# Kernel tuning notes

Hardware: AMD Instinct MI355X
Metric: run time of the kernel (lower is better)

## Reference

```python
import jax, jax.numpy as jnp
import numpy as np

N, E, D, EDIM, L, H = 50000, 800000, 128, 16, 3, 8


def setup_inputs() -> dict:
    key = jax.random.key(0)
    ks = jax.random.split(key, 16)
    inner = (L + 1) * D  # concat of input + 3 GCN layer outputs
    return {
        "x": jax.random.normal(ks[0], (N, D), jnp.float32),
        "edge_index": jax.random.randint(ks[1], (2, E), 0, N),
        "edge_attr": jax.random.normal(ks[2], (E, EDIM), jnp.float32),
        "dag_edge_index": jax.random.randint(ks[3], (2, E), 0, N),
        "W_v": jax.random.normal(ks[4], (D, D), jnp.float32) * 0.05,
        "W_qk": jax.random.normal(ks[5], (D, 2 * D), jnp.float32) * 0.05,
        "gcn_W": jax.random.normal(ks[6], (L, D, D), jnp.float32) * 0.05,
        "gcn_b": jnp.zeros((L, D), jnp.float32),
        "gcn_root": jax.random.normal(ks[7], (L, D), jnp.float32) * 0.05,
        "gcn_We": jax.random.normal(ks[8], (L, EDIM, D), jnp.float32) * 0.05,
        "gcn_be": jnp.zeros((L, D), jnp.float32),
        "bn_gamma": jnp.ones((inner,), jnp.float32),
        "bn_beta": jnp.zeros((inner,), jnp.float32),
        "W_se": jax.random.normal(ks[9], (inner, D), jnp.float32) * 0.05,
        "b_se": jnp.zeros((D,), jnp.float32),
        "W_out": jax.random.normal(ks[10], (D, D), jnp.float32) * 0.05,
        "b_out": jnp.zeros((D,), jnp.float32),
    }


def reference(x, edge_index, edge_attr, dag_edge_index, W_v, W_qk, gcn_W, gcn_b,
              gcn_root, gcn_We, gcn_be, bn_gamma, bn_beta, W_se, b_se, W_out, b_out):
    n = x.shape[0]
    row, col = edge_index[0], edge_index[1]  # source j, target i

    def gcn_layer(h, Wl, bl, root, We, be):
        h = h @ Wl + bl                                   # [N, D]
        e = edge_attr @ We + be                           # [E, D]
        deg = jax.ops.segment_sum(jnp.ones(row.shape[0], h.dtype), row, num_segments=n) + 1.0
        dis = deg ** -0.5
        norm = dis[row] * dis[col]                        # [E]
        msg = norm[:, None] * jax.nn.relu(h[row] + e)     # gather + per-edge transform
        agg = jax.ops.segment_sum(msg, col, num_segments=n)  # scatter-add at target
        return agg + jax.nn.relu(h + root) / deg[:, None]

    # StructureExtractor: 3 GCN layers, concat skip features
    xs = [x]
    h = x
    for i in range(gcn_W.shape[0]):
        h = jax.nn.relu(gcn_layer(h, gcn_W[i], gcn_b[i], gcn_root[i], gcn_We[i], gcn_be[i]))
        xs.append(h)
    xc = jnp.concatenate(xs, axis=-1)                     # [N, 4D]
    mu = xc.mean(0)
    var = xc.var(0)
    xc = (xc - mu) / jnp.sqrt(var + 1e-5) * bn_gamma + bn_beta  # BatchNorm1d (batch stats)
    x_struct = xc @ W_se + b_se                           # [N, D]

    # sparse multi-head attention over dag_rr_edge_index
    v = x @ W_v
    qk = x_struct @ W_qk
    d = x.shape[1]
    qk_src_tbl, qk_dst_tbl = qk[:, :d], qk[:, d:]         # chunk(2): (qk_j, qk_i)
    hd = d // H
    scale = hd ** -0.5
    src, dst = dag_edge_index[0], dag_edge_index[1]
    qj = qk_src_tbl[src].reshape(-1, H, hd)
    qi = qk_dst_tbl[dst].reshape(-1, H, hd)
    logits = (qi * qj).sum(-1) * scale                    # [E, H]
    m = jax.ops.segment_max(logits, dst, num_segments=n)
    p = jnp.exp(logits - m[dst])
    s = jax.ops.segment_sum(p, dst, num_segments=n)
    attn = p / s[dst]                                     # per-destination softmax
    vj = v[src].reshape(-1, H, hd)
    out = jax.ops.segment_sum(vj * attn[..., None], dst, num_segments=n).reshape(-1, d)
    return out @ W_out + b_out
```

## Files before the change

### kernel.cpp

```cpp
#include <hip/hip_runtime.h>

#define D 128
#define EDIMC 16
#define GCAP 64

typedef __attribute__((ext_vector_type(8))) short short8v;
typedef __attribute__((ext_vector_type(4))) float f32x4;
typedef __attribute__((ext_vector_type(2))) float f32x2;
typedef __attribute__((ext_vector_type(2))) _Float16 h16x2;

__device__ __forceinline__ float asf(unsigned u){ union{unsigned u; float f;} v; v.u = u; return v.f; }
__device__ __forceinline__ unsigned asu(float f){ union{float f; unsigned u;} v; v.f = f; return v.u; }
__device__ __forceinline__ unsigned short f2bf(float f){
    unsigned u = asu(f);
    unsigned r = (u + 0x7fffu + ((u >> 16) & 1u)) >> 16;
    return (unsigned short)r;
}
__device__ __forceinline__ unsigned packbf(float lo, float hi){
    return (unsigned)f2bf(lo) | ((unsigned)f2bf(hi) << 16);
}
__device__ __forceinline__ unsigned packh(float a, float b){
    union{ h16x2 h; unsigned u; } v;
    v.h = (h16x2){(_Float16)a, (_Float16)b};
    return v.u;
}
__device__ __forceinline__ h16x2 ash2(unsigned u){ union{unsigned u; h16x2 h;} v; v.u = u; return v.h; }

__global__ __launch_bounds__(256) void prep_all(
    const int* __restrict__ row, const int* __restrict__ col,
    const int* __restrict__ asrc_in, const int* __restrict__ adst,
    int E, int N, int gE, int gX, int L,
    const float* __restrict__ eattr, const float* __restrict__ x,
    const float* __restrict__ gW, const float* __restrict__ Wv,
    const float* __restrict__ Wqk, const float* __restrict__ Wout,
    const float* __restrict__ gWe, const float* __restrict__ bse,
    const float* __restrict__ Wse,
    int* __restrict__ cr, int* __restrict__ curg, int* __restrict__ curd,
    int2* __restrict__ gslot, int* __restrict__ asrcS, unsigned* __restrict__ eattrh,
    unsigned* __restrict__ xbf, unsigned* __restrict__ xc,
    unsigned short* __restrict__ gWt, unsigned short* __restrict__ Wvt,
    unsigned short* __restrict__ Woutt, unsigned* __restrict__ wpk,
    float* __restrict__ WseWqk, float* __restrict__ bconst)
{
    int b = blockIdx.x, tid = threadIdx.x;
    if(b < gE){
        int e = b*256 + tid;
        if(e >= E) return;
        const float4* s4 = (const float4*)(eattr + (size_t)e*EDIMC);
        float4 a = s4[0], bb = s4[1], cc2 = s4[2], d = s4[3];
        unsigned* dst8 = eattrh + (size_t)e*8;
        dst8[0] = packh(a.x, a.y);    dst8[1] = packh(a.z, a.w);
        dst8[2] = packh(bb.x, bb.y);  dst8[3] = packh(bb.z, bb.w);
        dst8[4] = packh(cc2.x, cc2.y);dst8[5] = packh(cc2.z, cc2.w);
        dst8[6] = packh(d.x, d.y);    dst8[7] = packh(d.z, d.w);
        int r = row[e], c = col[e];
        atomicAdd(&cr[r], 1);
        int pg = atomicAdd(&curg[c], 1);
        if(pg < GCAP) gslot[c*GCAP + pg] = make_int2(r, e);
        int s2 = asrc_in[e], d2 = adst[e];
        int pd = atomicAdd(&curd[d2], 1);
        if(pd < GCAP) asrcS[d2*GCAP + pd] = s2;
    } else if(b < gE + gX){
        int idx = (b - gE)*256 + tid;
        if(idx >= N*64) return;
        int i = idx >> 6, c2 = idx & 63;
        float a = x[(size_t)i*128 + c2*2], bb = x[(size_t)i*128 + c2*2 + 1];
        unsigned p = packbf(a, bb);
        xbf[idx] = p;
        xc[(size_t)i*256 + c2] = p;
    } else {
        int wb = b - gE - gX;
        int j = tid;
        if(wb < 384){
            int l = wb >> 7, k = wb & 127;
            if(j < 128) gWt[(size_t)l*16384 + (size_t)j*128 + k] = f2bf(gW[(size_t)l*16384 + (size_t)k*128 + j]);
        } else if(wb < 512){
            int k = wb - 384;
            if(j < 128) Wvt[(size_t)j*128 + k] = f2bf(Wv[(size_t)k*128 + j]);
        } else if(wb < 640){
            int k = wb - 512;
            if(j < 128) Woutt[(size_t)j*128 + k] = f2bf(Wout[(size_t)k*128 + j]);
        } else if(wb < 664){
            int t = wb - 640; int l = t >> 3, kk = t & 7;
            if(j < 128){
                const float* W = gWe + (size_t)l*EDIMC*D;
                wpk[(size_t)l*1024 + kk*128 + j] = packh(W[(size_t)(2*kk)*D + j], W[(size_t)(2*kk+1)*D + j]);
            }
        } else if(wb < 1176){
            int k = wb - 664;
            float acc = 0.f;
            #pragma unroll 4
            for(int c = 0; c < 128; c++)
                acc += Wse[(size_t)k*128 + c] * Wqk[(size_t)c*256 + j];
            WseWqk[(size_t)k*256 + j] = acc;
        } else {
            float acc = 0.f;
            #pragma unroll 4
            for(int c = 0; c < 128; c++)
                acc += bse[c] * Wqk[(size_t)c*256 + j];
            bconst[j] = acc;
        }
    }
}

__global__ void deg_fin2(const int* __restrict__ cr, float* __restrict__ deg,
                         float* __restrict__ dis, int N){
    int i = blockIdx.x*blockDim.x + threadIdx.x;
    if(i < N){ float d = (float)cr[i] + 1.0f; deg[i] = d; dis[i] = rsqrtf(d); }
}

template<int OUT>
__global__ __launch_bounds__(256) void gemm_lds(
    const unsigned short* __restrict__ A, const unsigned short* __restrict__ Bt,
    const float* __restrict__ bias, void* __restrict__ Cout,
    int M, int K, int Nc)
{
    __shared__ unsigned short As[128*64];
    __shared__ unsigned short Bs[128*64];
    int tid = threadIdx.x;
    int lane = tid & 63;
    int wid = tid >> 6;
    int bm = blockIdx.y*128, bn = blockIdx.x*128;
    int wr = (wid >> 1)*64, wc = (wid & 1)*64;
    int lr = lane & 15, kg = lane >> 4;
    f32x4 acc[4][4];
    #pragma unroll
    for(int i = 0; i < 4; i++)
        #pragma unroll
        for(int j = 0; j < 4; j++) acc[i][j] = (f32x4){0.f,0.f,0.f,0.f};

    for(int k0 = 0; k0 < K; k0 += 64){
        #pragma unroll
        for(int i = 0; i < 4; i++){
            int q = tid + 256*i;
            int row = q >> 3, c8 = (q & 7)*8;
            int ar = bm + row; if(ar >= M) ar = M - 1;
            *(short8v*)&As[row*64 + c8] = *(const short8v*)&A[(size_t)ar*K + k0 + c8];
            *(short8v*)&Bs[row*64 + c8] = *(const short8v*)&Bt[(size_t)(bn + row)*K + k0 + c8];
        }
        __syncthreads();
        #pragma unroll
        for(int kk = 0; kk < 2; kk++){
            short8v a[4], b[4];
            #pragma unroll
            for(int i = 0; i < 4; i++)
                a[i] = *(const short8v*)&As[(wr + i*16 + lr)*64 + kk*32 + kg*8];
            #pragma unroll
            for(int j = 0; j < 4; j++)
                b[j] = *(const short8v*)&Bs[(wc + j*16 + lr)*64 + kk*32 + kg*8];
            #pragma unroll
            for(int i = 0; i < 4; i++)
                #pragma unroll
                for(int j = 0; j < 4; j++)
                    acc[i][j] = __builtin_amdgcn_mfma_f32_16x16x32_bf16(a[i], b[j], acc[i][j], 0, 0, 0);
        }
        __syncthreads();
    }
    #pragma unroll
    for(int j = 0; j < 4; j++){
        int col = bn + wc + j*16 + lr;
        float bs = bias ? bias[col] : 0.f;
        #pragma unroll
        for(int i = 0; i < 4; i++){
            int rbase = bm + wr + i*16 + kg*4;
            #pragma unroll
            for(int r = 0; r < 4; r++){
                int rw = rbase + r;
                if(rw < M){
                    float val = acc[i][j][r] + bs;
                    if(OUT == 1)
                        ((unsigned short*)Cout)[(size_t)rw*Nc + col] = f2bf(val);
                    else if(OUT == 2)
                        ((_Float16*)Cout)[(size_t)rw*Nc + col] = (_Float16)val;
                    else
                        ((float*)Cout)[(size_t)rw*Nc + col] = val;
                }
            }
        }
    }
}

__device__ __forceinline__ void edge_acc5(
    uint4 ea0, uint4 ea1, unsigned hu, float nm,
    const unsigned* __restrict__ w0, const unsigned* __restrict__ w1,
    float be0, float be1, float& a0, float& a1)
{
    float ev0 = be0, ev1 = be1;
    unsigned ea[8] = {ea0.x, ea0.y, ea0.z, ea0.w, ea1.x, ea1.y, ea1.z, ea1.w};
    #pragma unroll
    for(int kk = 0; kk < 8; kk++){
        ev0 = __builtin_amdgcn_fdot2(ash2(ea[kk]), ash2(w0[kk]), ev0, false);
        ev1 = __builtin_amdgcn_fdot2(ash2(ea[kk]), ash2(w1[kk]), ev1, false);
    }
    float sx = fmaxf(asf(hu << 16) + ev0, 0.f);
    float sy = fmaxf(asf(hu & 0xffff0000u) + ev1, 0.f);
    a0 += nm*sx; a1 += nm*sy;
}

__global__ __launch_bounds__(256) void gcn_gather_v7(
    const unsigned* __restrict__ hlin, const int* __restrict__ curg,
    const int2* __restrict__ gslot, const unsigned* __restrict__ eattrh,
    const float* __restrict__ dis, const unsigned* __restrict__ wpk_l,
    const float* __restrict__ be, const float* __restrict__ root,
    const float* __restrict__ deg,
    unsigned* __restrict__ xc, unsigned* __restrict__ hcur, int blk, int N)
{
    int lane = threadIdx.x & 63;
    int node = __builtin_amdgcn_readfirstlane((int)((blockIdx.x*blockDim.x + threadIdx.x) >> 6));
    if(node >= N) return;
    unsigned w0[8], w1[8];
    const uint2* wp2 = (const uint2*)wpk_l;
    #pragma unroll
    for(int kk = 0; kk < 8; kk++){
        uint2 t = wp2[(size_t)kk*64 + lane];
        w0[kk] = t.x; w1[kk] = t.y;
    }
    f32x2 be2 = ((const f32x2*)be)[lane];
    f32x2 rt2 = ((const f32x2*)root)[lane];
    float disn = dis[node];
    int s0 = node*GCAP;
    int s1 = s0 + min(curg[node], GCAP);
    float a0 = 0.f, a1 = 0.f;
    int s = s0;
    for(; s + 4 <= s1; s += 4){
        int2 sl0 = gslot[s+0], sl1 = gslot[s+1], sl2 = gslot[s+2], sl3 = gslot[s+3];
        float d0 = dis[sl0.x], d1 = dis[sl1.x], d2 = dis[sl2.x], d3 = dis[sl3.x];
        unsigned h0 = hlin[(size_t)sl0.x*64 + lane];
        unsigned h1 = hlin[(size_t)sl1.x*64 + lane];
        unsigned h2 = hlin[(size_t)sl2.x*64 + lane];
        unsigned h3 = hlin[(size_t)sl3.x*64 + lane];
        uint4 e00 = *(const uint4*)(eattrh + (size_t)sl0.y*8);
        uint4 e01 = *(const uint4*)(eattrh + (size_t)sl0.y*8 + 4);
        uint4 e10 = *(const uint4*)(eattrh + (size_t)sl1.y*8);
        uint4 e11 = *(const uint4*)(eattrh + (size_t)sl1.y*8 + 4);
        uint4 e20 = *(const uint4*)(eattrh + (size_t)sl2.y*8);
        uint4 e21 = *(const uint4*)(eattrh + (size_t)sl2.y*8 + 4);
        uint4 e30 = *(const uint4*)(eattrh + (size_t)sl3.y*8);
        uint4 e31 = *(const uint4*)(eattrh + (size_t)sl3.y*8 + 4);
        edge_acc5(e00, e01, h0, d0*disn, w0, w1, be2.x, be2.y, a0, a1);
        edge_acc5(e10, e11, h1, d1*disn, w0, w1, be2.x, be2.y, a0, a1);
        edge_acc5(e20, e21, h2, d2*disn, w0, w1, be2.x, be2.y, a0, a1);
        edge_acc5(e30, e31, h3, d3*disn, w0, w1, be2.x, be2.y, a0, a1);
    }
    for(; s < s1; s++){
        int2 sl0 = gslot[s];
        float d0 = dis[sl0.x];
        unsigned h0 = hlin[(size_t)sl0.x*64 + lane];
        uint4 e00 = *(const uint4*)(eattrh + (size_t)sl0.y*8);
        uint4 e01 = *(const uint4*)(eattrh + (size_t)sl0.y*8 + 4);
        edge_acc5(e00, e01, h0, d0*disn, w0, w1, be2.x, be2.y, a0, a1);
    }
    unsigned hlu = hlin[(size_t)node*64 + lane];
    float hlx = asf(hlu << 16), hly = asf(hlu & 0xffff0000u);
    float dinv = 1.f/deg[node];
    float v0 = fmaxf(a0 + fmaxf(hlx + rt2.x, 0.f)*dinv, 0.f);
    float v1 = fmaxf(a1 + fmaxf(hly + rt2.y, 0.f)*dinv, 0.f);
    unsigned p = packbf(v0, v1);
    hcur[(size_t)node*64 + lane] = p;
    xc[(size_t)node*256 + (size_t)blk*64 + lane] = p;
}

__global__ __launch_bounds__(256) void bn_stats_bf(
    const unsigned* __restrict__ xc, int N, float* __restrict__ stats)
{
    int c0 = threadIdx.x;
    int rows_per = (N + gridDim.x - 1)/gridDim.x;
    int r0 = blockIdx.x*rows_per, r1 = min(N, r0 + rows_per);
    float s0=0, q0=0, s1=0, q1=0;
    for(int r = r0; r < r1; r++){
        unsigned u = xc[(size_t)r*256 + c0];
        float a = asf(u << 16), b = asf(u & 0xffff0000u);
        s0 += a; q0 += a*a; s1 += b; q1 += b*b;
    }
    atomicAdd(&stats[2*c0+0], s0);  atomicAdd(&stats[512 + 2*c0+0], q0);
    atomicAdd(&stats[2*c0+1], s1);  atomicAdd(&stats[512 + 2*c0+1], q1);
}

__global__ void fold_all(const float* __restrict__ gamma, const float* __restrict__ beta,
                         const float* __restrict__ stats, float Ninv,
                         const float* __restrict__ WseWqk, const float* __restrict__ bconst,
                         unsigned short* __restrict__ Wqkft, float* __restrict__ bqkf)
{
    int b = blockIdx.x, t = threadIdx.x;
    if(b < 256){
        int j = b;
        #pragma unroll
        for(int half = 0; half < 2; half++){
            int k = t + half*256;
            float mu  = stats[k]*Ninv;
            float var = stats[512+k]*Ninv - mu*mu;
            float sc  = gamma[k]*rsqrtf(var + 1e-5f);
            Wqkft[(size_t)j*512 + k] = f2bf(sc * WseWqk[(size_t)k*256 + j]);
        }
    } else {
        int j = t;
        float acc = bconst[j];
        for(int k = 0; k < 512; k++){
            float mu  = stats[k]*Ninv;
            float var = stats[512+k]*Ninv - mu*mu;
            float sc  = gamma[k]*rsqrtf(var + 1e-5f);
            float sh  = beta[k] - mu*sc;
            acc += sh*WseWqk[(size_t)k*256 + j];
        }
        bqkf[j] = acc;
    }
}

__global__ __launch_bounds__(256) void attn_fused_v8(
    const unsigned* __restrict__ qk, const unsigned* __restrict__ v,
    const int* __restrict__ curd, const int* __restrict__ asrcS,
    unsigned* __restrict__ out, int N)
{
    int lane = threadIdx.x & 63;
    int node = __builtin_amdgcn_readfirstlane((int)((blockIdx.x*blockDim.x + threadIdx.x) >> 6));
    if(node >= N) return;
    int cnt = min(curd[node], GCAP);
    int s0 = node*GCAP, s1 = s0 + cnt;
    float o0 = 0.f, o1 = 0.f;
    if(cnt > 0){
        h16x2 qi2 = ash2(qk[(size_t)node*128 + 64 + lane]);
        float m = -INFINITY, ssum = 0.f, a0 = 0.f, a1 = 0.f;
        int s = s0;
        for(; s + 4 <= s1; s += 4){
            int sr0 = asrcS[s+0], sr1 = asrcS[s+1], sr2 = asrcS[s+2], sr3 = asrcS[s+3];
            unsigned qj[4], vv[4];
            qj[0] = qk[(size_t)sr0*128 + lane];  vv[0] = v[(size_t)sr0*64 + lane];
            qj[1] = qk[(size_t)sr1*128 + lane];  vv[1] = v[(size_t)sr1*64 + lane];
            qj[2] = qk[(size_t)sr2*128 + lane];  vv[2] = v[(size_t)sr2*64 + lane];
            qj[3] = qk[(size_t)sr3*128 + lane];  vv[3] = v[(size_t)sr3*64 + lane];
            float l[4];
            #pragma unroll
            for(int j = 0; j < 4; j++){
                float p = __builtin_amdgcn_fdot2(qi2, ash2(qj[j]), 0.f, false);
                p += __shfl_xor(p, 1);
                p += __shfl_xor(p, 2);
                p += __shfl_xor(p, 4);
                l[j] = p*0.25f;
            }
            float mc = fmaxf(fmaxf(fmaxf(l[0], l[1]), fmaxf(l[2], l[3])), m);
            float sc = __expf(m - mc);
            float p0 = __expf(l[0] - mc), p1 = __expf(l[1] - mc);
            float p2 = __expf(l[2] - mc), p3 = __expf(l[3] - mc);
            h16x2 v0 = ash2(vv[0]), v1 = ash2(vv[1]), v2 = ash2(vv[2]), v3 = ash2(vv[3]);
            ssum = ssum*sc + (p0 + p1 + p2 + p3);
            a0 = a0*sc + p0*(float)v0.x + p1*(float)v1.x + p2*(float)v2.x + p3*(float)v3.x;
            a1 = a1*sc + p0*(float)v0.y + p1*(float)v1.y + p2*(float)v2.y + p3*(float)v3.y;
            m = mc;
        }
        for(; s < s1; s++){
            int srx = asrcS[s];
            h16x2 qj2 = ash2(qk[(size_t)srx*128 + lane]);
            h16x2 v2  = ash2(v [(size_t)srx*64  + lane]);
            float p = __builtin_amdgcn_fdot2(qi2, qj2, 0.f, false);
            p += __shfl_xor(p, 1);
            p += __shfl_xor(p, 2);
            p += __shfl_xor(p, 4);
            float l = p*0.25f;
            float mn = fmaxf(m, l);
            float sc = __expf(m - mn);
            float pe = __expf(l - mn);
            ssum = ssum*sc + pe;
            a0 = a0*sc + pe*(float)v2.x;
            a1 = a1*sc + pe*(float)v2.y;
            m = mn;
        }
        float inv = 1.f/ssum;
        o0 = a0*inv; o1 = a1*inv;
    }
    out[(size_t)node*64 + lane] = packbf(o0, o1);
}

extern "C" void kernel_launch(void* const* d_in, const int* in_sizes, int n_in,
                              void* d_out, int out_size, void* d_ws, size_t ws_size,
                              hipStream_t stream)
{
    const float* x     = (const float*)d_in[0];
    const int*   ei    = (const int*)  d_in[1];
    const float* eattr = (const float*)d_in[2];
    const int*   dei   = (const int*)  d_in[3];
    const float* Wv    = (const float*)d_in[4];
    const float* Wqk   = (const float*)d_in[5];
    const float* gW    = (const float*)d_in[6];
    const float* gb    = (const float*)d_in[7];
    const float* groot = (const float*)d_in[8];
    const float* gWe   = (const float*)d_in[9];
    const float* gbe   = (const float*)d_in[10];
    const float* gamma = (const float*)d_in[11];
    const float* beta  = (const float*)d_in[12];
    const float* Wse   = (const float*)d_in[13];
    const float* bse   = (const float*)d_in[14];
    const float* Wout  = (const float*)d_in[15];
    const float* bout  = (const float*)d_in[16];

    const int N = in_sizes[0]/D;
    const int E = in_sizes[1]/2;
    const int L = in_sizes[7]/D;

    float* ws = (float*)d_ws;
    size_t o = 0;
    auto alloc = [&](size_t n){ size_t r = o; o += (n + 63) & ~(size_t)63; return r; };
    size_t f_deg   = alloc((size_t)N);
    size_t f_dis   = alloc((size_t)N);
    size_t f_hlin  = alloc((size_t)N*64);
    size_t f_hcur  = alloc((size_t)N*64);
    size_t f_xbf   = alloc((size_t)N*64);
    size_t f_xc    = alloc((size_t)N*256);
    size_t f_st    = alloc(1024);
    size_t f_cnt   = alloc((size_t)N*3);
    size_t f_gslot = alloc((size_t)N*GCAP*2);
    size_t f_asrc  = alloc((size_t)N*GCAP);
    size_t f_eah   = alloc((size_t)E*8);
    size_t f_wgt   = alloc(40960 + 64);
    size_t f_wpk   = alloc(3*1024);
    size_t f_wsq   = alloc(512*256);
    size_t f_bcn   = alloc(256);
    size_t f_wqf   = alloc(65536);
    size_t f_bqf   = alloc(256);
    size_t f_qk    = alloc((size_t)N*128);
    size_t f_vb    = alloc((size_t)N*64);
    size_t f_aout  = alloc((size_t)N*64);
    (void)ws_size;

    float* deg  = ws + f_deg;   float* dis  = ws + f_dis;
    unsigned* hlin = (unsigned*)(ws + f_hlin);
    unsigned* hcur = (unsigned*)(ws + f_hcur);
    unsigned* xbf  = (unsigned*)(ws + f_xbf);
    unsigned* xc   = (unsigned*)(ws + f_xc);
    float* stats = ws + f_st;
    int* cnts = (int*)(ws + f_cnt);
    int* cr = cnts, *curg = cnts + N, *curd = cnts + 2*N;
    int2* gslot = (int2*)(ws + f_gslot);
    int* asrcS = (int*)(ws + f_asrc);
    unsigned* eattrh = (unsigned*)(ws + f_eah);
    unsigned short* wbase = (unsigned short*)(ws + f_wgt);
    unsigned short* gWt   = wbase;
    unsigned short* Wvt   = gWt + 3*128*128;
    unsigned short* Woutt = Wvt + 128*128;
    unsigned* wpk = (unsigned*)(ws + f_wpk);
    float* WseWqk = ws + f_wsq;
    float* bconst = ws + f_bcn;
    unsigned short* Wqkft = (unsigned short*)(ws + f_wqf);
    float* bqkf = ws + f_bqf;
    unsigned* qk   = (unsigned*)(ws + f_qk);
    unsigned* vbuf = (unsigned*)(ws + f_vb);
    unsigned* aout = (unsigned*)(ws + f_aout);

    const int* e_row = ei;        const int* e_col = ei + E;
    const int* a_src = dei;       const int* a_dst = dei + E;

    dim3 blk256(256);
    int gE = (E+255)/256, gN = (N+255)/256;
    int gNode = ((size_t)N*64 + 255)/256;
    int gX = gNode;
    int gM128 = (N+127)/128;

    hipMemsetAsync(cnts, 0, (size_t)N*3*sizeof(int), stream);
    prep_all<<<gE + gX + 1177, blk256, 0, stream>>>(
        e_row, e_col, a_src, a_dst, E, N, gE, gX, L,
        eattr, x, gW, Wv, Wqk, Wout, gWe, bse, Wse,
        cr, curg, curd, gslot, asrcS, eattrh,
        xbf, xc, gWt, Wvt, Woutt, wpk, WseWqk, bconst);
    deg_fin2<<<gN, blk256, 0, stream>>>(cr, deg, dis, N);

    const unsigned* hin = xbf;
    for(int l = 0; l < L; l++){
        dim3 g(1, gM128);
        gemm_lds<1><<<g, blk256, 0, stream>>>((const unsigned short*)hin, gWt + (size_t)l*D*D,
                                              gb + (size_t)l*D, hlin, N, 128, 128);
        gcn_gather_v7<<<gNode, blk256, 0, stream>>>(hlin, curg, gslot, eattrh, dis,
                                                    wpk + (size_t)l*1024, gbe + (size_t)l*D,
                                                    groot + (size_t)l*D, deg, xc, hcur, l+1, N);
        hin = hcur;
    }

    hipMemsetAsync(stats, 0, 1024*sizeof(float), stream);
    bn_stats_bf<<<1024, blk256, 0, stream>>>(xc, N, stats);
    float Ninv = 1.0f/(float)N;
    fold_all<<<257, blk256, 0, stream>>>(gamma, beta, stats, Ninv, WseWqk, bconst, Wqkft, bqkf);

    {   dim3 g(1, gM128);
        gemm_lds<2><<<g, blk256, 0, stream>>>((const unsigned short*)xbf, Wvt, nullptr, vbuf, N, 128, 128);
    }
    {   dim3 g(2, gM128);
        gemm_lds<2><<<g, blk256, 0, stream>>>((const unsigned short*)xc, Wqkft, bqkf, qk, N, 512, 256);
    }

    attn_fused_v8<<<gNode, blk256, 0, stream>>>(qk, vbuf, curd, asrcS, aout, N);

    {   dim3 g(1, gM128);
        gemm_lds<0><<<g, blk256, 0, stream>>>((const unsigned short*)aout, Woutt, bout, (float*)d_out, N, 128, 128);
    }
}
```

Before: 620.5 us.

## Unroll edge gathers to 8 and move Wse·Wqk fold onto matrix-core GEMM

The GCN gather and attention loops now process 8 neighbours per iteration instead of 4, so more independent gather loads are in flight per wave to hide memory latency. The 512x256 Wse·Wqk weight product, previously a scalar fp32 loop inside prep_all, is now computed by converting both matrices to bf16 and running the existing LDS GEMM kernel. This removes a long serial tail from the prep kernel. In exchange it adds a kernel launch, lowers that product to bf16 precision, and raises register pressure in the unrolled loops.

```diff
diff --git a/kernel.cpp b/kernel.cpp
--- a/kernel.cpp
+++ b/kernel.cpp
@@ -40,7 +40,8 @@
     unsigned* __restrict__ xbf, unsigned* __restrict__ xc,
     unsigned short* __restrict__ gWt, unsigned short* __restrict__ Wvt,
     unsigned short* __restrict__ Woutt, unsigned* __restrict__ wpk,
-    float* __restrict__ WseWqk, float* __restrict__ bconst)
+    unsigned short* __restrict__ Wse_bf, unsigned short* __restrict__ Wqkt2,
+    float* __restrict__ bconst)
 {
     int b = blockIdx.x, tid = threadIdx.x;
     if(b < gE){
@@ -86,13 +87,12 @@
                 const float* W = gWe + (size_t)l*EDIMC*D;
                 wpk[(size_t)l*1024 + kk*128 + j] = packh(W[(size_t)(2*kk)*D + j], W[(size_t)(2*kk+1)*D + j]);
             }
-        } else if(wb < 1176){
-            int k = wb - 664;
-            float acc = 0.f;
-            #pragma unroll 4
-            for(int c = 0; c < 128; c++)
-                acc += Wse[(size_t)k*128 + c] * Wqk[(size_t)c*256 + j];
-            WseWqk[(size_t)k*256 + j] = acc;
+        } else if(wb < 920){
+            int idx = (wb - 664)*256 + j;
+            Wse_bf[idx] = f2bf(Wse[idx]);
+        } else if(wb < 1048){
+            int c = wb - 920;
+            Wqkt2[(size_t)j*128 + c] = f2bf(Wqk[(size_t)c*256 + j]);
         } else {
             float acc = 0.f;
             #pragma unroll 4
@@ -197,7 +197,7 @@
     a0 += nm*sx; a1 += nm*sy;
 }
 
-__global__ __launch_bounds__(256) void gcn_gather_v7(
+__global__ __launch_bounds__(256) void gcn_gather_v9(
     const unsigned* __restrict__ hlin, const int* __restrict__ curg,
     const int2* __restrict__ gslot, const unsigned* __restrict__ eattrh,
     const float* __restrict__ dis, const unsigned* __restrict__ wpk_l,
@@ -222,25 +222,22 @@
     int s1 = s0 + min(curg[node], GCAP);
     float a0 = 0.f, a1 = 0.f;
     int s = s0;
-    for(; s + 4 <= s1; s += 4){
-        int2 sl0 = gslot[s+0], sl1 = gslot[s+1], sl2 = gslot[s+2], sl3 = gslot[s+3];
-        float d0 = dis[sl0.x], d1 = dis[sl1.x], d2 = dis[sl2.x], d3 = dis[sl3.x];
-        unsigned h0 = hlin[(size_t)sl0.x*64 + lane];
-        unsigned h1 = hlin[(size_t)sl1.x*64 + lane];
-        unsigned h2 = hlin[(size_t)sl2.x*64 + lane];
-        unsigned h3 = hlin[(size_t)sl3.x*64 + lane];
-        uint4 e00 = *(const uint4*)(eattrh + (size_t)sl0.y*8);
-        uint4 e01 = *(const uint4*)(eattrh + (size_t)sl0.y*8 + 4);
-        uint4 e10 = *(const uint4*)(eattrh + (size_t)sl1.y*8);
-        uint4 e11 = *(const uint4*)(eattrh + (size_t)sl1.y*8 + 4);
-        uint4 e20 = *(const uint4*)(eattrh + (size_t)sl2.y*8);
-        uint4 e21 = *(const uint4*)(eattrh + (size_t)sl2.y*8 + 4);
-        uint4 e30 = *(const uint4*)(eattrh + (size_t)sl3.y*8);
-        uint4 e31 = *(const uint4*)(eattrh + (size_t)sl3.y*8 + 4);
-        edge_acc5(e00, e01, h0, d0*disn, w0, w1, be2.x, be2.y, a0, a1);
-        edge_acc5(e10, e11, h1, d1*disn, w0, w1, be2.x, be2.y, a0, a1);
-        edge_acc5(e20, e21, h2, d2*disn, w0, w1, be2.x, be2.y, a0, a1);
-        edge_acc5(e30, e31, h3, d3*disn, w0, w1, be2.x, be2.y, a0, a1);
+    for(; s + 8 <= s1; s += 8){
+        int2 sl[8];
+        #pragma unroll
+        for(int j = 0; j < 8; j++) sl[j] = gslot[s+j];
+        float dd[8]; unsigned hh[8];
+        #pragma unroll
+        for(int j = 0; j < 8; j++){
+            dd[j] = dis[sl[j].x];
+            hh[j] = hlin[(size_t)sl[j].x*64 + lane];
+        }
+        #pragma unroll
+        for(int j = 0; j < 8; j++){
+            uint4 e0 = *(const uint4*)(eattrh + (size_t)sl[j].y*8);
+            uint4 e1 = *(const uint4*)(eattrh + (size_t)sl[j].y*8 + 4);
+            edge_acc5(e0, e1, hh[j], dd[j]*disn, w0, w1, be2.x, be2.y, a0, a1);
+        }
     }
     for(; s < s1; s++){
         int2 sl0 = gslot[s];
@@ -306,7 +303,7 @@
     }
 }
 
-__global__ __launch_bounds__(256) void attn_fused_v8(
+__global__ __launch_bounds__(256) void attn_fused_v9(
     const unsigned* __restrict__ qk, const unsigned* __restrict__ v,
     const int* __restrict__ curd, const int* __restrict__ asrcS,
     unsigned* __restrict__ out, int N)
@@ -321,30 +318,41 @@
         h16x2 qi2 = ash2(qk[(size_t)node*128 + 64 + lane]);
         float m = -INFINITY, ssum = 0.f, a0 = 0.f, a1 = 0.f;
         int s = s0;
-        for(; s + 4 <= s1; s += 4){
-            int sr0 = asrcS[s+0], sr1 = asrcS[s+1], sr2 = asrcS[s+2], sr3 = asrcS[s+3];
-            unsigned qj[4], vv[4];
-            qj[0] = qk[(size_t)sr0*128 + lane];  vv[0] = v[(size_t)sr0*64 + lane];
-            qj[1] = qk[(size_t)sr1*128 + lane];  vv[1] = v[(size_t)sr1*64 + lane];
-            qj[2] = qk[(size_t)sr2*128 + lane];  vv[2] = v[(size_t)sr2*64 + lane];
-            qj[3] = qk[(size_t)sr3*128 + lane];  vv[3] = v[(size_t)sr3*64 + lane];
-            float l[4];
-            #pragma unroll
-            for(int j = 0; j < 4; j++){
+        for(; s + 8 <= s1; s += 8){
+            int sr[8];
+            #pragma unroll
+            for(int j = 0; j < 8; j++) sr[j] = asrcS[s+j];
+            unsigned qj[8], vv[8];
+            #pragma unroll
+            for(int j = 0; j < 8; j++){
+                qj[j] = qk[(size_t)sr[j]*128 + lane];
+                vv[j] = v [(size_t)sr[j]*64  + lane];
+            }
+            float l[8];
+            #pragma unroll
+            for(int j = 0; j < 8; j++){
                 float p = __builtin_amdgcn_fdot2(qi2, ash2(qj[j]), 0.f, false);
                 p += __shfl_xor(p, 1);
                 p += __shfl_xor(p, 2);
                 p += __shfl_xor(p, 4);
                 l[j] = p*0.25f;
             }
-            float mc = fmaxf(fmaxf(fmaxf(l[0], l[1]), fmaxf(l[2], l[3])), m);
+            float mc = m;
+            #pragma unroll
+            for(int j = 0; j < 8; j++) mc = fmaxf(mc, l[j]);
             float sc = __expf(m - mc);
-            float p0 = __expf(l[0] - mc), p1 = __expf(l[1] - mc);
-            float p2 = __expf(l[2] - mc), p3 = __expf(l[3] - mc);
-            h16x2 v0 = ash2(vv[0]), v1 = ash2(vv[1]), v2 = ash2(vv[2]), v3 = ash2(vv[3]);
-            ssum = ssum*sc + (p0 + p1 + p2 + p3);
-            a0 = a0*sc + p0*(float)v0.x + p1*(float)v1.x + p2*(float)v2.x + p3*(float)v3.x;
-            a1 = a1*sc + p0*(float)v0.y + p1*(float)v1.y + p2*(float)v2.y + p3*(float)v3.y;
+            float psum = 0.f, av0 = 0.f, av1 = 0.f;
+            #pragma unroll
+            for(int j = 0; j < 8; j++){
+                float p = __expf(l[j] - mc);
+                h16x2 v2 = ash2(vv[j]);
+                psum += p;
+                av0 += p*(float)v2.x;
+                av1 += p*(float)v2.y;
+            }
+            ssum = ssum*sc + psum;
+            a0 = a0*sc + av0;
+            a1 = a1*sc + av1;
             m = mc;
         }
         for(; s < s1; s++){
@@ -412,6 +420,8 @@
     size_t f_eah   = alloc((size_t)E*8);
     size_t f_wgt   = alloc(40960 + 64);
     size_t f_wpk   = alloc(3*1024);
+    size_t f_wsebf = alloc(32768 + 64);
+    size_t f_wqt2  = alloc(16384 + 64);
     size_t f_wsq   = alloc(512*256);
     size_t f_bcn   = alloc(256);
     size_t f_wqf   = alloc(65536);
@@ -437,6 +447,8 @@
     unsigned short* Wvt   = gWt + 3*128*128;
     unsigned short* Woutt = Wvt + 128*128;
     unsigned* wpk = (unsigned*)(ws + f_wpk);
+    unsigned short* Wse_bf = (unsigned short*)(ws + f_wsebf);
+    unsigned short* Wqkt2  = (unsigned short*)(ws + f_wqt2);
     float* WseWqk = ws + f_wsq;
     float* bconst = ws + f_bcn;
     unsigned short* Wqkft = (unsigned short*)(ws + f_wqf);
@@ -455,19 +467,23 @@
     int gM128 = (N+127)/128;
 
     hipMemsetAsync(cnts, 0, (size_t)N*3*sizeof(int), stream);
-    prep_all<<<gE + gX + 1177, blk256, 0, stream>>>(
+    prep_all<<<gE + gX + 1049, blk256, 0, stream>>>(
         e_row, e_col, a_src, a_dst, E, N, gE, gX, L,
         eattr, x, gW, Wv, Wqk, Wout, gWe, bse, Wse,
         cr, curg, curd, gslot, asrcS, eattrh,
-        xbf, xc, gWt, Wvt, Woutt, wpk, WseWqk, bconst);
+        xbf, xc, gWt, Wvt, Woutt, wpk, Wse_bf, Wqkt2, bconst);
     deg_fin2<<<gN, blk256, 0, stream>>>(cr, deg, dis, N);
+
+    {   dim3 g(2, 4);
+        gemm_lds<0><<<g, blk256, 0, stream>>>(Wse_bf, Wqkt2, nullptr, WseWqk, 512, 128, 256);
+    }
 
     const unsigned* hin = xbf;
     for(int l = 0; l < L; l++){
         dim3 g(1, gM128);
         gemm_lds<1><<<g, blk256, 0, stream>>>((const unsigned short*)hin, gWt + (size_t)l*D*D,
                                               gb + (size_t)l*D, hlin, N, 128, 128);
-        gcn_gather_v7<<<gNode, blk256, 0, stream>>>(hlin, curg, gslot, eattrh, dis,
+        gcn_gather_v9<<<gNode, blk256, 0, stream>>>(hlin, curg, gslot, eattrh, dis,
                                                     wpk + (size_t)l*1024, gbe + (size_t)l*D,
                                                     groot + (size_t)l*D, deg, xc, hcur, l+1, N);
         hin = hcur;
@@ -485,7 +501,7 @@
         gemm_lds<2><<<g, blk256, 0, stream>>>((const unsigned short*)xc, Wqkft, bqkf, qk, N, 512, 256);
     }
 
-    attn_fused_v8<<<gNode, blk256, 0, stream>>>(qk, vbuf, curd, asrcS, aout, N);
+    attn_fused_v9<<<gNode, blk256, 0, stream>>>(qk, vbuf, curd, asrcS, aout, N);
 
     {   dim3 g(1, gM128);
         gemm_lds<0><<<g, blk256, 0, stream>>>((const unsigned short*)aout, Woutt, bout, (float*)d_out, N, 128, 128);
```

New measurement: 640.2 us. 3.2% more time.

## Split each node's edge list across four wavefronts in GCN gather and attention

Applied to the files above, without the earlier changes.

The GCN gather and sparse attention kernels now give each node its own 256-thread block instead of one wavefront, and each of the four waves handles a quarter of the node's edges. Partial sums are combined through shared memory after a block barrier. Attention partials carry a running max so the online softmax can be merged across waves. This shortens the serial per-wave edge loop and exposes more memory-level parallelism. In exchange it adds a barrier and LDS traffic per node, leaves three idle waves during the epilogue, and loads the per-layer weights redundantly in each wave.

```diff
diff --git a/kernel.cpp b/kernel.cpp
--- a/kernel.cpp
+++ b/kernel.cpp
@@ -197,7 +197,7 @@
     a0 += nm*sx; a1 += nm*sy;
 }
 
-__global__ __launch_bounds__(256) void gcn_gather_v7(
+__global__ __launch_bounds__(256) void gcn_gather_v10(
     const unsigned* __restrict__ hlin, const int* __restrict__ curg,
     const int2* __restrict__ gslot, const unsigned* __restrict__ eattrh,
     const float* __restrict__ dis, const unsigned* __restrict__ wpk_l,
@@ -205,9 +205,11 @@
     const float* __restrict__ deg,
     unsigned* __restrict__ xc, unsigned* __restrict__ hcur, int blk, int N)
 {
-    int lane = threadIdx.x & 63;
-    int node = __builtin_amdgcn_readfirstlane((int)((blockIdx.x*blockDim.x + threadIdx.x) >> 6));
-    if(node >= N) return;
+    __shared__ float part[4][64][2];
+    int tid = threadIdx.x;
+    int lane = tid & 63;
+    int h = __builtin_amdgcn_readfirstlane(tid >> 6);
+    int node = blockIdx.x;
     unsigned w0[8], w1[8];
     const uint2* wp2 = (const uint2*)wpk_l;
     #pragma unroll
@@ -216,10 +218,11 @@
         w0[kk] = t.x; w1[kk] = t.y;
     }
     f32x2 be2 = ((const f32x2*)be)[lane];
-    f32x2 rt2 = ((const f32x2*)root)[lane];
     float disn = dis[node];
-    int s0 = node*GCAP;
-    int s1 = s0 + min(curg[node], GCAP);
+    int cnt = min(curg[node], GCAP);
+    int base = node*GCAP;
+    int q0 = (cnt*h) >> 2, q1 = (cnt*(h+1)) >> 2;
+    int s0 = base + q0, s1 = base + q1;
     float a0 = 0.f, a1 = 0.f;
     int s = s0;
     for(; s + 4 <= s1; s += 4){
@@ -250,14 +253,22 @@
         uint4 e01 = *(const uint4*)(eattrh + (size_t)sl0.y*8 + 4);
         edge_acc5(e00, e01, h0, d0*disn, w0, w1, be2.x, be2.y, a0, a1);
     }
-    unsigned hlu = hlin[(size_t)node*64 + lane];
-    float hlx = asf(hlu << 16), hly = asf(hlu & 0xffff0000u);
-    float dinv = 1.f/deg[node];
-    float v0 = fmaxf(a0 + fmaxf(hlx + rt2.x, 0.f)*dinv, 0.f);
-    float v1 = fmaxf(a1 + fmaxf(hly + rt2.y, 0.f)*dinv, 0.f);
-    unsigned p = packbf(v0, v1);
-    hcur[(size_t)node*64 + lane] = p;
-    xc[(size_t)node*256 + (size_t)blk*64 + lane] = p;
+    part[h][lane][0] = a0;
+    part[h][lane][1] = a1;
+    __syncthreads();
+    if(h == 0){
+        a0 = part[0][lane][0] + part[1][lane][0] + part[2][lane][0] + part[3][lane][0];
+        a1 = part[0][lane][1] + part[1][lane][1] + part[2][lane][1] + part[3][lane][1];
+        f32x2 rt2 = ((const f32x2*)root)[lane];
+        unsigned hlu = hlin[(size_t)node*64 + lane];
+        float hlx = asf(hlu << 16), hly = asf(hlu & 0xffff0000u);
+        float dinv = 1.f/deg[node];
+        float v0 = fmaxf(a0 + fmaxf(hlx + rt2.x, 0.f)*dinv, 0.f);
+        float v1 = fmaxf(a1 + fmaxf(hly + rt2.y, 0.f)*dinv, 0.f);
+        unsigned p = packbf(v0, v1);
+        hcur[(size_t)node*64 + lane] = p;
+        xc[(size_t)node*256 + (size_t)blk*64 + lane] = p;
+    }
 }
 
 __global__ __launch_bounds__(256) void bn_stats_bf(
@@ -306,20 +317,23 @@
     }
 }
 
-__global__ __launch_bounds__(256) void attn_fused_v8(
+__global__ __launch_bounds__(256) void attn_fused_v10(
     const unsigned* __restrict__ qk, const unsigned* __restrict__ v,
     const int* __restrict__ curd, const int* __restrict__ asrcS,
     unsigned* __restrict__ out, int N)
 {
-    int lane = threadIdx.x & 63;
-    int node = __builtin_amdgcn_readfirstlane((int)((blockIdx.x*blockDim.x + threadIdx.x) >> 6));
-    if(node >= N) return;
+    __shared__ float4 part[4][64];
+    int tid = threadIdx.x;
+    int lane = tid & 63;
+    int h = __builtin_amdgcn_readfirstlane(tid >> 6);
+    int node = blockIdx.x;
     int cnt = min(curd[node], GCAP);
-    int s0 = node*GCAP, s1 = s0 + cnt;
-    float o0 = 0.f, o1 = 0.f;
+    int base = node*GCAP;
+    int q0 = (cnt*h) >> 2, q1 = (cnt*(h+1)) >> 2;
+    int s0 = base + q0, s1 = base + q1;
+    float m = -INFINITY, ssum = 0.f, a0 = 0.f, a1 = 0.f;
     if(cnt > 0){
         h16x2 qi2 = ash2(qk[(size_t)node*128 + 64 + lane]);
-        float m = -INFINITY, ssum = 0.f, a0 = 0.f, a1 = 0.f;
         int s = s0;
         for(; s + 4 <= s1; s += 4){
             int sr0 = asrcS[s+0], sr1 = asrcS[s+1], sr2 = asrcS[s+2], sr3 = asrcS[s+3];
@@ -364,10 +378,24 @@
             a1 = a1*sc + pe*(float)v2.y;
             m = mn;
         }
-        float inv = 1.f/ssum;
-        o0 = a0*inv; o1 = a1*inv;
-    }
-    out[(size_t)node*64 + lane] = packbf(o0, o1);
+    }
+    part[h][lane] = make_float4(m, ssum, a0, a1);
+    __syncthreads();
+    if(h == 0){
+        float o0 = 0.f, o1 = 0.f;
+        if(cnt > 0){
+            float4 p0 = part[0][lane], p1 = part[1][lane], p2 = part[2][lane], p3 = part[3][lane];
+            float mm = fmaxf(fmaxf(p0.x, p1.x), fmaxf(p2.x, p3.x));
+            float w0 = __expf(p0.x - mm), w1 = __expf(p1.x - mm);
+            float w2 = __expf(p2.x - mm), w3 = __expf(p3.x - mm);
+            float ss = p0.y*w0 + p1.y*w1 + p2.y*w2 + p3.y*w3;
+            float b0 = p0.z*w0 + p1.z*w1 + p2.z*w2 + p3.z*w3;
+            float b1 = p0.w*w0 + p1.w*w1 + p2.w*w2 + p3.w*w3;
+            float inv = 1.f/ss;
+            o0 = b0*inv; o1 = b1*inv;
+        }
+        out[(size_t)node*64 + lane] = packbf(o0, o1);
+    }
 }
 
 extern "C" void kernel_launch(void* const* d_in, const int* in_sizes, int n_in,
@@ -467,9 +495,9 @@
         dim3 g(1, gM128);
         gemm_lds<1><<<g, blk256, 0, stream>>>((const unsigned short*)hin, gWt + (size_t)l*D*D,
                                               gb + (size_t)l*D, hlin, N, 128, 128);
-        gcn_gather_v7<<<gNode, blk256, 0, stream>>>(hlin, curg, gslot, eattrh, dis,
-                                                    wpk + (size_t)l*1024, gbe + (size_t)l*D,
-                                                    groot + (size_t)l*D, deg, xc, hcur, l+1, N);
+        gcn_gather_v10<<<N, blk256, 0, stream>>>(hlin, curg, gslot, eattrh, dis,
+                                                 wpk + (size_t)l*1024, gbe + (size_t)l*D,
+                                                 groot + (size_t)l*D, deg, xc, hcur, l+1, N);
         hin = hcur;
     }
 
@@ -485,7 +513,7 @@
         gemm_lds<2><<<g, blk256, 0, stream>>>((const unsigned short*)xc, Wqkft, bqkf, qk, N, 512, 256);
     }
 
-    attn_fused_v8<<<gNode, blk256, 0, stream>>>(qk, vbuf, curd, asrcS, aout, N);
+    attn_fused_v10<<<N, blk256, 0, stream>>>(qk, vbuf, curd, asrcS, aout, N);
 
     {   dim3 g(1, gM128);
         gemm_lds<0><<<g, blk256, 0, stream>>>((const unsigned short*)aout, Woutt, bout, (float*)d_out, N, 128, 128);
```

Result: slower. 678.3 us (+9.3%).
